# Optimization experiments

Hardware: AMD Instinct MI355X
Metric: run time of the kernel (lower is better)

Reference implementation:

```python
import jax, jax.numpy as jnp
import numpy as np

EPS = 1e-5
H, W, C, NCLS = 8, 16, 64, 8

def _bn_params(key, c):
    k1, k2, k3, k4 = jax.random.split(key, 4)
    gamma = jax.random.uniform(k1, (c,), minval=0.5, maxval=1.5)
    beta = 0.1 * jax.random.normal(k2, (c,))
    mean = 0.1 * jax.random.normal(k3, (c,))
    var = jax.random.uniform(k4, (c,), minval=0.5, maxval=1.5)
    return jnp.stack([gamma, beta, mean, var]).astype(jnp.float32)  # (4, c)

def bn2d(x, p):
    # eval-mode BatchNorm2d; p: (4, C); x: (B, C, H, W)
    g, b, m, v = p[0], p[1], p[2], p[3]
    s = g * jax.lax.rsqrt(v + EPS)
    return x * s[None, :, None, None] + (b - m * s)[None, :, None, None]

def bn1d_scalar(x, p):
    # eval-mode BatchNorm1d with 1 channel; p: (4, 1); x: (B, 1, F)
    g, b, m, v = p[0], p[1], p[2], p[3]
    s = g * jax.lax.rsqrt(v + EPS)
    return x * s + (b - m * s)

def conv_same(x, w, b):
    y = jax.lax.conv_general_dilated(x, w, (1, 1), 'SAME',
                                     dimension_numbers=('NCHW', 'OIHW', 'NCHW'))
    return y + b[None, :, None, None]

def setup_inputs() -> dict:
    key = jax.random.key(0)
    ks = jax.random.split(key, 24)
    B = 8192
    d = {}
    d['x'] = jax.random.normal(ks[0], (B, 1, H, W), dtype=jnp.float32)
    d['bn0'] = _bn_params(ks[1], 1)
    d['conv1_w'] = 0.1 * jax.random.normal(ks[2], (C, 1, 3, 3), dtype=jnp.float32)
    d['conv1_b'] = jnp.zeros((C,), jnp.float32)
    d['bn1'] = _bn_params(ks[3], C)
    d['conv2_w'] = (0.1 / np.sqrt(C)) * jax.random.normal(ks[4], (C, C, 3, 3), dtype=jnp.float32)
    d['conv2_b'] = jnp.zeros((C,), jnp.float32)
    d['bn2'] = _bn_params(ks[5], C)
    # LocallyConnected2d, kernel_size=1 -> per-pixel (out_c, in_c) weights
    d['lc3_w'] = (1.0 / np.sqrt(C)) * jax.random.normal(ks[6], (C, C, H, W), dtype=jnp.float32)
    d['bn3'] = _bn_params(ks[7], C)
    d['lc4_w'] = (1.0 / np.sqrt(C)) * jax.random.normal(ks[8], (C, C, H, W), dtype=jnp.float32)
    d['bn4'] = _bn_params(ks[9], C)
    F5 = H * W * C
    d['fc5_w'] = (1.0 / np.sqrt(F5)) * jax.random.normal(ks[10], (512, F5), dtype=jnp.float32)
    d['fc5_b'] = jnp.zeros((512,), jnp.float32)
    d['bn5'] = _bn_params(ks[11], 1)
    d['fc6_w'] = (1.0 / np.sqrt(512)) * jax.random.normal(ks[12], (512, 512), dtype=jnp.float32)
    d['fc6_b'] = jnp.zeros((512,), jnp.float32)
    d['bn6'] = _bn_params(ks[13], 1)
    d['fc7_w'] = (1.0 / np.sqrt(512)) * jax.random.normal(ks[14], (128, 512), dtype=jnp.float32)
    d['fc7_b'] = jnp.zeros((128,), jnp.float32)
    d['bn7'] = _bn_params(ks[15], 1)
    d['fc8_w'] = (1.0 / np.sqrt(128)) * jax.random.normal(ks[16], (NCLS, 128), dtype=jnp.float32)
    d['fc8_b'] = jnp.zeros((NCLS,), jnp.float32)
    return d

def reference(x, bn0, conv1_w, conv1_b, bn1, conv2_w, conv2_b, bn2,
              lc3_w, bn3, lc4_w, bn4, fc5_w, fc5_b, bn5,
              fc6_w, fc6_b, bn6, fc7_w, fc7_b, bn7, fc8_w, fc8_b):
    B = x.shape[0]
    # squeeze -> view(B, 16, 8) -> transpose(1,2) -> add channel dim
    h = jnp.swapaxes(x.reshape(B, W, H), 1, 2)[:, None]  # (B,1,H,W)
    h = bn2d(h, bn0)
    h = jax.nn.relu(bn2d(conv_same(h, conv1_w, conv1_b), bn1))
    h = jax.nn.relu(bn2d(conv_same(h, conv2_w, conv2_b), bn2))
    # locally connected, k=1: per-pixel channel mixing
    h = jax.nn.relu(bn2d(jnp.einsum('bchw,ochw->bohw', h, lc3_w), bn3))
    h = jax.nn.relu(bn2d(jnp.einsum('bchw,ochw->bohw', h, lc4_w), bn4))
    h = h.reshape(B, 1, -1)  # (B, 1, C*H*W)
    h = h @ fc5_w.T + fc5_b
    h = jax.nn.relu(bn1d_scalar(h, bn5))
    h = jax.nn.relu(bn1d_scalar(h @ fc6_w.T + fc6_b, bn6))
    h = jax.nn.relu(bn1d_scalar(h @ fc7_w.T + fc7_b, bn7))
    h = h @ fc8_w.T + fc8_b
    return h.reshape(B, NCLS)
```

## Files before the change

### kernel.cpp

```cpp
#include <hip/hip_runtime.h>
#include <hip/hip_bf16.h>

typedef unsigned short bf16_t;
typedef __attribute__((ext_vector_type(8))) short bf16x8;
typedef __attribute__((ext_vector_type(8))) unsigned short u16x8;
typedef __attribute__((ext_vector_type(4))) float f32x4;

#if defined(__has_builtin)
#if __has_builtin(__builtin_amdgcn_global_load_lds)
#define HAS_GLL 1
#endif
#endif

__device__ __forceinline__ float b2f(bf16_t u) {
    return __uint_as_float(((unsigned int)u) << 16);
}
__device__ __forceinline__ bf16_t f2b(float f) {
    unsigned int x = __float_as_uint(f);
    unsigned int r = x + 0x7fffu + ((x >> 16) & 1u);
    return (bf16_t)(r >> 16);
}
__device__ __forceinline__ unsigned int pk2(float a, float b) {
    __hip_bfloat162 t = __float22bfloat162_rn(make_float2(a, b));
    return *(unsigned int*)&t;
}
__device__ __forceinline__ float ldf(const void* p, int i, int isf) {
    return isf ? ((const float*)p)[i] : b2f(((const bf16_t*)p)[i]);
}

__device__ __forceinline__ void stg16(const bf16_t* g, bf16_t* l) {
#ifdef HAS_GLL
    __builtin_amdgcn_global_load_lds(
        (const __attribute__((address_space(1))) unsigned int*)g,
        (__attribute__((address_space(3))) unsigned int*)l,
        16, 0, 0);
#else
    *(uint4*)l = *(const uint4*)g;
#endif
}

#define OFF_S0T0 0
#define OFF_W1   16
#define OFF_S1   592
#define OFF_H1   656
#define OFF_S2   720
#define OFF_H2   784
#define OFF_S3   848
#define OFF_H3   912
#define OFF_S4   976
#define OFF_H4   1040
#define OFF_SC5  1104
#define OFF_H5   1112
#define OFF_SC6  1624
#define OFF_H6   1632
#define OFF_SC7  2144
#define OFF_H7   2152
#define OFF_W8   2280
#define OFF_B8   3304
#define OFF_FLAG 4032

__global__ __launch_bounds__(256) void setup_kernel(
    const void* __restrict__ w2, const void* __restrict__ w3,
    const void* __restrict__ w4, const void* __restrict__ w5,
    const void* __restrict__ w6, const void* __restrict__ w7,
    bf16_t* __restrict__ w2p, bf16_t* __restrict__ w3p,
    bf16_t* __restrict__ w4p, bf16_t* __restrict__ w5p,
    bf16_t* __restrict__ w6b, bf16_t* __restrict__ w7b,
    const float* __restrict__ prm)
{
    const int isf = prm[OFF_FLAG] > 0.5f;
    const int i = blockIdx.x * 256 + threadIdx.x;
    if (i < 36864) {
        int oc = i / 576, r = i - oc * 576;
        int tap = r >> 6, ic = r & 63;
        w2p[i] = f2b(ldf(w2, oc * 576 + ic * 9 + tap, isf));
    } else if (i < 561152) {
        int j = i - 36864;
        int p = j >> 12, r = j & 4095;
        int oc = r >> 6, ic = r & 63;
        w3p[j] = f2b(ldf(w3, oc * 8192 + ic * 128 + p, isf));
    } else if (i < 1085440) {
        int j = i - 561152;
        int p = j >> 12, r = j & 4095;
        int oc = r >> 6, ic = r & 63;
        w4p[j] = f2b(ldf(w4, oc * 8192 + ic * 128 + p, isf));
    } else if (i < 5279744) {
        int j = i - 1085440;
        int nr = j >> 13, r = j & 8191;
        int p = r >> 6, c = r & 63;
        w5p[j] = f2b(ldf(w5, nr * 8192 + c * 128 + p, isf));
    } else if (i < 5541888) {
        int j = i - 5279744;
        w6b[j] = isf ? f2b(((const float*)w6)[j]) : ((const bf16_t*)w6)[j];
    } else if (i < 5607424) {
        int j = i - 5541888;
        w7b[j] = isf ? f2b(((const float*)w7)[j]) : ((const bf16_t*)w7)[j];
    }
}

__global__ __launch_bounds__(256) void fold_params_kernel(
    const void* xraw,
    const void* bn0p, const void* w1, const void* b1, const void* bn1p,
    const void* b2c, const void* bn2p, const void* bn3p, const void* bn4p,
    const void* b5, const void* bn5p, const void* b6, const void* bn6p,
    const void* b7, const void* bn7p, const void* w8, const void* b8,
    float* prm)
{
    __shared__ float sflag;
    const int t = threadIdx.x;
    if (t == 0) {
        const unsigned int* w = (const unsigned int*)xraw;
        int good = 0;
        for (int i = 0; i < 64; i++) {
            float f = __uint_as_float(w[i] << 16);
            float a = fabsf(f);
            if (a >= 0.0009765625f && a <= 16.0f) good++;
        }
        float fl = (good >= 32) ? 0.0f : 1.0f;
        sflag = fl;
        prm[OFF_FLAG] = fl;
    }
    __syncthreads();
    const int isf = sflag > 0.5f;

    if (t == 0) {
        float g = ldf(bn0p, 0, isf), be = ldf(bn0p, 1, isf);
        float m = ldf(bn0p, 2, isf), v = ldf(bn0p, 3, isf);
        float s = g * rsqrtf(v + 1e-5f);
        prm[OFF_S0T0] = s; prm[OFF_S0T0 + 1] = be - m * s;
    }
    for (int i = t; i < 576; i += 256) prm[OFF_W1 + i] = ldf(w1, i, isf);

    if (t < 64) {
        {
            float g = ldf(bn1p, t, isf), be = ldf(bn1p, 64 + t, isf);
            float m = ldf(bn1p, 128 + t, isf), v = ldf(bn1p, 192 + t, isf);
            float s = g * rsqrtf(v + 1e-5f);
            prm[OFF_S1 + t] = s;
            prm[OFF_H1 + t] = s * ldf(b1, t, isf) + (be - m * s);
        }
        {
            float g = ldf(bn2p, t, isf), be = ldf(bn2p, 64 + t, isf);
            float m = ldf(bn2p, 128 + t, isf), v = ldf(bn2p, 192 + t, isf);
            float s = g * rsqrtf(v + 1e-5f);
            prm[OFF_S2 + t] = s;
            prm[OFF_H2 + t] = s * ldf(b2c, t, isf) + (be - m * s);
        }
        {
            float g = ldf(bn3p, t, isf), be = ldf(bn3p, 64 + t, isf);
            float m = ldf(bn3p, 128 + t, isf), v = ldf(bn3p, 192 + t, isf);
            float s = g * rsqrtf(v + 1e-5f);
            prm[OFF_S3 + t] = s;
            prm[OFF_H3 + t] = be - m * s;
        }
        {
            float g = ldf(bn4p, t, isf), be = ldf(bn4p, 64 + t, isf);
            float m = ldf(bn4p, 128 + t, isf), v = ldf(bn4p, 192 + t, isf);
            float s = g * rsqrtf(v + 1e-5f);
            prm[OFF_S4 + t] = s;
            prm[OFF_H4 + t] = be - m * s;
        }
    }
    {
        float g = ldf(bn5p, 0, isf), be = ldf(bn5p, 1, isf);
        float m = ldf(bn5p, 2, isf), v = ldf(bn5p, 3, isf);
        float s = g * rsqrtf(v + 1e-5f);
        if (t == 0) prm[OFF_SC5] = s;
        for (int i = t; i < 512; i += 256)
            prm[OFF_H5 + i] = s * ldf(b5, i, isf) + (be - m * s);
    }
    {
        float g = ldf(bn6p, 0, isf), be = ldf(bn6p, 1, isf);
        float m = ldf(bn6p, 2, isf), v = ldf(bn6p, 3, isf);
        float s = g * rsqrtf(v + 1e-5f);
        if (t == 0) prm[OFF_SC6] = s;
        for (int i = t; i < 512; i += 256)
            prm[OFF_H6 + i] = s * ldf(b6, i, isf) + (be - m * s);
    }
    {
        float g = ldf(bn7p, 0, isf), be = ldf(bn7p, 1, isf);
        float m = ldf(bn7p, 2, isf), v = ldf(bn7p, 3, isf);
        float s = g * rsqrtf(v + 1e-5f);
        if (t == 0) prm[OFF_SC7] = s;
        if (t < 128) prm[OFF_H7 + t] = s * ldf(b7, t, isf) + (be - m * s);
    }
    for (int i = t; i < 1024; i += 256) prm[OFF_W8 + i] = ldf(w8, i, isf);
    if (t < 8) prm[OFF_B8 + t] = ldf(b8, t, isf);
}

__global__ __launch_bounds__(256) void conv1_kernel(
    const void* __restrict__ x, const float* __restrict__ prm,
    bf16_t* __restrict__ c1, int Bc, int c0)
{
    __shared__ float xn[180];
    __shared__ float w1s[576];

    const int t = threadIdx.x;
    const int b0 = blockIdx.x * 4;
    const int isf = prm[OFF_FLAG] > 0.5f;
    const float s0 = prm[OFF_S0T0], t0 = prm[OFF_S0T0 + 1];

    for (int i = t; i < 576; i += 256) w1s[i] = prm[OFF_W1 + i];

    const int pg  = t & 31;
    const int oc0 = (t >> 5) * 8;

    float s1[8], h1[8];
    #pragma unroll
    for (int j = 0; j < 8; j++) {
        s1[j] = prm[OFF_S1 + oc0 + j];
        h1[j] = prm[OFF_H1 + oc0 + j];
    }

    for (int s = 0; s < 4; s++) {
        const int b = b0 + s;
        __syncthreads();
        if (t < 180) {
            int row = t / 18, col = t - row * 18;
            float v = 0.f;
            if (row >= 1 && row <= 8 && col >= 1 && col <= 16)
                v = s0 * ldf(x, (c0 + b) * 128 + (col - 1) * 8 + (row - 1), isf) + t0;
            xn[t] = v;
        }
        __syncthreads();

        #pragma unroll
        for (int m = 0; m < 4; m++) {
            int p = pg + 32 * m;
            int h = p >> 4, w = p & 15;
            float r[9];
            #pragma unroll
            for (int dh = 0; dh < 3; dh++)
                #pragma unroll
                for (int dw = 0; dw < 3; dw++)
                    r[dh * 3 + dw] = xn[(h + dh) * 18 + (w + dw)];
            u16x8 o;
            #pragma unroll
            for (int j = 0; j < 8; j++) {
                float acc = 0.f;
                #pragma unroll
                for (int k = 0; k < 9; k++) acc += r[k] * w1s[(oc0 + j) * 9 + k];
                o[j] = f2b(fmaxf(s1[j] * acc + h1[j], 0.f));
            }
            *(u16x8*)(c1 + (size_t)p * Bc * 64 + (size_t)b * 64 + oc0) = o;
        }
    }
}

__global__ __launch_bounds__(256) void fused_mfma_kernel(
    const bf16_t* __restrict__ c1, const bf16_t* __restrict__ w2p,
    const bf16_t* __restrict__ w3p, const bf16_t* __restrict__ w4p,
    const float* __restrict__ prm, bf16_t* __restrict__ bufA, int Bc)
{
    __shared__ bf16_t sm[20480];
    const int t    = threadIdx.x;
    const int lane = t & 63;
    const int wv   = t >> 6;
    const int m0   = blockIdx.x * 256;
    const int p    = blockIdx.y;
    const int h    = p >> 4, w = p & 15;

    const int fr = lane & 15;
    const int fg = lane >> 4;
    const int swz4 = (fr >> 1) & 3;

    const int gS    = (t & 3) ^ ((t >> 3) & 3);
    const int rA    = t >> 2;
    const int coff0 = rA * 64 + gS * 8;
    const int w2off = rA * 576 + gS * 8;

    u16x8 wr3[2], wr4[2];
    {
        const bf16_t* w3b = w3p + (size_t)p * 4096 + coff0;
        const bf16_t* w4b = w4p + (size_t)p * 4096 + coff0;
        wr3[0] = *(const u16x8*)(w3b);
        wr3[1] = *(const u16x8*)(w3b + 32);
        wr4[0] = *(const u16x8*)(w4b);
        wr4[1] = *(const u16x8*)(w4b + 32);
    }

    f32x4 acc[4][4];
    #pragma unroll
    for (int i = 0; i < 4; i++)
        #pragma unroll
        for (int j = 0; j < 4; j++)
            acc[i][j] = (f32x4){0.f, 0.f, 0.f, 0.f};

    const bf16_t* c1b = c1 + (size_t)m0 * 64 + coff0;
    const size_t planeStride = (size_t)Bc * 64;

    {
        if (h > 0 && w > 0) {
            const bf16_t* ab = c1b + (size_t)((h - 1) * 16 + (w - 1)) * planeStride;
            #pragma unroll
            for (int u = 0; u < 4; u++)
                stg16(ab + u * 4096, sm + t * 8 + u * 2048);
            stg16(w2p + w2off, sm + 16384 + t * 8);
        }
    }
    #pragma unroll
    for (int s = 0; s < 18; s++) {
        const int cur = s & 1;
        __syncthreads();
        if (s + 1 < 18) {
            const int s1  = s + 1;
            const int tap = s1 >> 1;
            const int dh = tap / 3 - 1, dw = tap % 3 - 1;
            const int hh = h + dh, ww = w + dw;
            if (hh >= 0 && hh < 8 && ww >= 0 && ww < 16) {
                const int nb  = cur ^ 1;
                const int ic0 = (s1 & 1) * 32;
                const bf16_t* ab = c1b + (size_t)(hh * 16 + ww) * planeStride + ic0;
                #pragma unroll
                for (int u = 0; u < 4; u++)
                    stg16(ab + u * 4096, sm + nb * 8192 + t * 8 + u * 2048);
                stg16(w2p + w2off + tap * 64 + ic0, sm + 16384 + nb * 2048 + t * 8);
            }
        }
        {
            const int tap = s >> 1;
            const int dh = tap / 3 - 1, dw = tap % 3 - 1;
            const int hh = h + dh, ww = w + dw;
            if (hh >= 0 && hh < 8 && ww >= 0 && ww < 16) {
                const bf16_t* Ab = sm + cur * 8192;
                const bf16_t* Bb = sm + 16384 + cur * 2048;
                bf16x8 hf[4], wf[4];
                #pragma unroll
                for (int j = 0; j < 4; j++)
                    hf[j] = *(const bf16x8*)(Ab + ((wv * 64 + j * 16 + fr) * 4 + (fg ^ swz4)) * 8);
                #pragma unroll
                for (int i = 0; i < 4; i++)
                    wf[i] = *(const bf16x8*)(Bb + ((i * 16 + fr) * 4 + (fg ^ swz4)) * 8);
                #pragma unroll
                for (int i = 0; i < 4; i++)
                    #pragma unroll
                    for (int j = 0; j < 4; j++)
                        acc[i][j] = __builtin_amdgcn_mfma_f32_16x16x32_bf16(
                            wf[i], hf[j], acc[i][j], 0, 0, 0);
            }
        }
    }
    __syncthreads();

#define EPILOGUE(SOFF, HOFF)                                                  \
    _Pragma("unroll")                                                         \
    for (int i = 0; i < 4; i++) {                                             \
        const int oc0e = i * 16 + fg * 4;                                     \
        const float4 sv = *(const float4*)(prm + (SOFF) + oc0e);              \
        const float4 hv = *(const float4*)(prm + (HOFF) + oc0e);              \
        _Pragma("unroll")                                                     \
        for (int j = 0; j < 4; j++) {                                         \
            const int bi = wv * 64 + j * 16 + fr;                             \
            float v0 = fmaxf(sv.x * acc[i][j][0] + hv.x, 0.f);                \
            float v1 = fmaxf(sv.y * acc[i][j][1] + hv.y, 0.f);                \
            float v2 = fmaxf(sv.z * acc[i][j][2] + hv.z, 0.f);                \
            float v3 = fmaxf(sv.w * acc[i][j][3] + hv.w, 0.f);                \
            uint2 pk; pk.x = pk2(v0, v1); pk.y = pk2(v2, v3);                 \
            *(uint2*)(sm + bi * 72 + oc0e) = pk;                              \
        }                                                                     \
    }

    EPILOGUE(OFF_S2, OFF_H2)
    *(u16x8*)(sm + 18432 + t * 8) = wr3[0];
    __syncthreads();

    #pragma unroll
    for (int i = 0; i < 4; i++)
        #pragma unroll
        for (int j = 0; j < 4; j++)
            acc[i][j] = (f32x4){0.f, 0.f, 0.f, 0.f};

    #pragma unroll
    for (int ks = 0; ks < 2; ks++) {
        if (ks == 1) {
            __syncthreads();
            *(u16x8*)(sm + 18432 + t * 8) = wr3[1];
            __syncthreads();
        }
        bf16x8 hf[4], wf[4];
        #pragma unroll
        for (int j = 0; j < 4; j++)
            hf[j] = *(const bf16x8*)(sm + (wv * 64 + j * 16 + fr) * 72 + ks * 32 + fg * 8);
        #pragma unroll
        for (int i = 0; i < 4; i++)
            wf[i] = *(const bf16x8*)(sm + 18432 + ((i * 16 + fr) * 4 + (fg ^ swz4)) * 8);
        #pragma unroll
        for (int i = 0; i < 4; i++)
            #pragma unroll
            for (int j = 0; j < 4; j++)
                acc[i][j] = __builtin_amdgcn_mfma_f32_16x16x32_bf16(
                    wf[i], hf[j], acc[i][j], 0, 0, 0);
    }

    EPILOGUE(OFF_S3, OFF_H3)
    __syncthreads();
    *(u16x8*)(sm + 18432 + t * 8) = wr4[0];
    __syncthreads();

    #pragma unroll
    for (int i = 0; i < 4; i++)
        #pragma unroll
        for (int j = 0; j < 4; j++)
            acc[i][j] = (f32x4){0.f, 0.f, 0.f, 0.f};

    #pragma unroll
    for (int ks = 0; ks < 2; ks++) {
        if (ks == 1) {
            __syncthreads();
            *(u16x8*)(sm + 18432 + t * 8) = wr4[1];
            __syncthreads();
        }
        bf16x8 hf[4], wf[4];
        #pragma unroll
        for (int j = 0; j < 4; j++)
            hf[j] = *(const bf16x8*)(sm + (wv * 64 + j * 16 + fr) * 72 + ks * 32 + fg * 8);
        #pragma unroll
        for (int i = 0; i < 4; i++)
            wf[i] = *(const bf16x8*)(sm + 18432 + ((i * 16 + fr) * 4 + (fg ^ swz4)) * 8);
        #pragma unroll
        for (int i = 0; i < 4; i++)
            #pragma unroll
            for (int j = 0; j < 4; j++)
                acc[i][j] = __builtin_amdgcn_mfma_f32_16x16x32_bf16(
                    wf[i], hf[j], acc[i][j], 0, 0, 0);
    }

    EPILOGUE(OFF_S4, OFF_H4)
#undef EPILOGUE
    __syncthreads();

    const int wrow = t >> 3, wc0 = (t & 7) * 8;
    #pragma unroll
    for (int pass = 0; pass < 8; pass++) {
        const int row = wrow + pass * 32;
        *(uint4*)(bufA + (size_t)(m0 + row) * 8192 + p * 64 + wc0) =
            *(const uint4*)(sm + row * 72 + wc0);
    }
}

__global__ __launch_bounds__(256) void gemm_mfma(
    const bf16_t* __restrict__ A, const bf16_t* __restrict__ W,
    const float* __restrict__ prm, int sc_off, int sh_off,
    bf16_t* __restrict__ out, int K, int N)
{
    __shared__ bf16_t sm[24576];
    const int t    = threadIdx.x;
    const int lane = t & 63;
    const int wv   = t >> 6;
    const int wr   = wv >> 1, wc = wv & 1;
    const int m0   = blockIdx.x * 128, n0 = blockIdx.y * 64;

    const int fr = lane & 15;
    const int fg = lane >> 4;
    const int swz8 = fr & 7;

    const bf16_t* srcA[4]; bf16_t* dstA[4];
    #pragma unroll
    for (int u = 0; u < 4; u++) {
        const int c = t + 256 * u;
        const int row = c >> 3;
        const int g = (c & 7) ^ (row & 7);
        srcA[u] = A + (size_t)(m0 + row) * K + g * 8;
        dstA[u] = sm + c * 8;
    }
    const bf16_t* srcB[2]; bf16_t* dstB[2];
    #pragma unroll
    for (int u = 0; u < 2; u++) {
        const int c = t + 256 * u;
        const int row = c >> 3;
        const int g = (c & 7) ^ (row & 7);
        srcB[u] = W + (size_t)(n0 + row) * K + g * 8;
        dstB[u] = sm + 16384 + c * 8;
    }

    f32x4 acc[4][2];
    #pragma unroll
    for (int i = 0; i < 4; i++)
        #pragma unroll
        for (int j = 0; j < 2; j++)
            acc[i][j] = (f32x4){0.f, 0.f, 0.f, 0.f};

    const int KS = K >> 6;

    #pragma unroll
    for (int u = 0; u < 4; u++) stg16(srcA[u], dstA[u]);
    #pragma unroll
    for (int u = 0; u < 2; u++) stg16(srcB[u], dstB[u]);

    for (int ks = 0; ks < KS; ks++) {
        const int cur = ks & 1;
        __syncthreads();
        if (ks + 1 < KS) {
            const int nb = cur ^ 1;
            const int kk = (ks + 1) << 6;
            #pragma unroll
            for (int u = 0; u < 4; u++) stg16(srcA[u] + kk, dstA[u] + nb * 8192);
            #pragma unroll
            for (int u = 0; u < 2; u++) stg16(srcB[u] + kk, dstB[u] + nb * 4096);
        }
        const bf16_t* Ab = sm + cur * 8192;
        const bf16_t* Bb = sm + 16384 + cur * 4096;
        bf16x8 af[4][2], bf2[2][2];
        #pragma unroll
        for (int i = 0; i < 4; i++)
            #pragma unroll
            for (int hh = 0; hh < 2; hh++) {
                const int r = wr * 64 + i * 16 + fr;
                const int g = hh * 4 + fg;
                af[i][hh] = *(const bf16x8*)(Ab + (r * 8 + (g ^ swz8)) * 8);
            }
        #pragma unroll
        for (int j = 0; j < 2; j++)
            #pragma unroll
            for (int hh = 0; hh < 2; hh++) {
                const int r = wc * 32 + j * 16 + fr;
                const int g = hh * 4 + fg;
                bf2[j][hh] = *(const bf16x8*)(Bb + (r * 8 + (g ^ swz8)) * 8);
            }
        #pragma unroll
        for (int hh = 0; hh < 2; hh++)
            #pragma unroll
            for (int i = 0; i < 4; i++)
                #pragma unroll
                for (int j = 0; j < 2; j++)
                    acc[i][j] = __builtin_amdgcn_mfma_f32_16x16x32_bf16(
                        af[i][hh], bf2[j][hh], acc[i][j], 0, 0, 0);
    }

    const float s    = prm[sc_off];
    const int   orow = fg * 4;
    const int   ocol = fr;
    #pragma unroll
    for (int j = 0; j < 2; j++) {
        const int n  = n0 + wc * 32 + j * 16 + ocol;
        const float sh = prm[sh_off + n];
        #pragma unroll
        for (int i = 0; i < 4; i++) {
            const int mb = m0 + wr * 64 + i * 16 + orow;
            #pragma unroll
            for (int r = 0; r < 4; r++) {
                float v = fmaxf(s * acc[i][j][r] + sh, 0.f);
                out[(size_t)(mb + r) * N + n] = f2b(v);
            }
        }
    }
}

__global__ __launch_bounds__(256) void fc8_kernel(
    const bf16_t* __restrict__ h, const float* __restrict__ prm,
    void* __restrict__ out, int c0)
{
    __shared__ float wsm[8 * 129];
    const int t = threadIdx.x;
    for (int i = t; i < 1024; i += 256) {
        int n = i >> 7, k = i & 127;
        wsm[n * 129 + k] = prm[OFF_W8 + i];
    }
    __syncthreads();
    const int isf = prm[OFF_FLAG] > 0.5f;
    const int bl = t >> 3, n = t & 7;
    const int b = c0 + blockIdx.x * 32 + bl;
    const bf16_t* hb = h + (size_t)(blockIdx.x * 32 + bl) * 128;
    float acc = prm[OFF_B8 + n];
    for (int k = 0; k < 128; k++) acc += b2f(hb[k]) * wsm[n * 129 + k];
    if (isf) ((float*)out)[(size_t)b * 8 + n] = acc;
    else     ((bf16_t*)out)[(size_t)b * 8 + n] = f2b(acc);
}

extern "C" void kernel_launch(void* const* d_in, const int* in_sizes, int n_in,
                              void* d_out, int out_size, void* d_ws, size_t ws_size,
                              hipStream_t stream)
{
    const void* x    = d_in[0];
    const void* bn0p = d_in[1];
    const void* w1   = d_in[2];
    const void* b1   = d_in[3];
    const void* bn1p = d_in[4];
    const void* w2   = d_in[5];
    const void* b2c  = d_in[6];
    const void* bn2p = d_in[7];
    const void* w3   = d_in[8];
    const void* bn3p = d_in[9];
    const void* w4   = d_in[10];
    const void* bn4p = d_in[11];
    const void* w5   = d_in[12];
    const void* b5   = d_in[13];
    const void* bn5p = d_in[14];
    const void* w6   = d_in[15];
    const void* b6   = d_in[16];
    const void* bn6p = d_in[17];
    const void* w7   = d_in[18];
    const void* b7   = d_in[19];
    const void* bn7p = d_in[20];
    const void* w8   = d_in[21];
    const void* b8   = d_in[22];

    char* base = (char*)d_ws;
    float*  prm = (float*)(base + 0);
    bf16_t* w2p = (bf16_t*)(base + 16384);
    bf16_t* w3p = (bf16_t*)(base + 90112);
    bf16_t* w4p = (bf16_t*)(base + 1138688);
    bf16_t* w5p = (bf16_t*)(base + 2187264);
    bf16_t* w6b = (bf16_t*)(base + 10575872);
    bf16_t* w7b = (bf16_t*)(base + 11100160);
    char*   acts = base + 11231232;

    const int B = 8192;
    const size_t FIXED = 11231232ull;

    fold_params_kernel<<<1, 256, 0, stream>>>(
        x, bn0p, w1, b1, bn1p, b2c, bn2p, bn3p, bn4p,
        b5, bn5p, b6, bn6p, b7, bn7p, w8, b8, prm);
    setup_kernel<<<21904, 256, 0, stream>>>(
        w2, w3, w4, w5, w6, w7, w2p, w3p, w4p, w5p, w6b, w7b, prm);

    const int Bf = 4096;
    const size_t FULL_NEED = FIXED + (size_t)Bf * 16384ull + (size_t)B * 18688ull;

    if (ws_size >= FULL_NEED) {
        bf16_t* c1   = (bf16_t*)acts;
        bf16_t* bufA = c1 + (size_t)Bf * 8192;
        bf16_t* bufC = bufA + (size_t)B * 8192;
        bf16_t* bufD = bufC + (size_t)B * 512;
        bf16_t* bufE = bufD + (size_t)B * 512;

        for (int c0 = 0; c0 < B; c0 += Bf) {
            conv1_kernel<<<Bf / 4, 256, 0, stream>>>(x, prm, c1, Bf, c0);
            fused_mfma_kernel<<<dim3(Bf / 256, 128), 256, 0, stream>>>(
                c1, w2p, w3p, w4p, prm, bufA + (size_t)c0 * 8192, Bf);
        }
        gemm_mfma<<<dim3(B / 128, 8), 256, 0, stream>>>(
            bufA, w5p, prm, OFF_SC5, OFF_H5, bufC, 8192, 512);
        gemm_mfma<<<dim3(B / 128, 8), 256, 0, stream>>>(
            bufC, w6b, prm, OFF_SC6, OFF_H6, bufD, 512, 512);
        gemm_mfma<<<dim3(B / 128, 2), 256, 0, stream>>>(
            bufD, w7b, prm, OFF_SC7, OFF_H7, bufE, 512, 128);
        fc8_kernel<<<B / 32, 256, 0, stream>>>(bufE, prm, d_out, 0);
    } else {
        size_t avail = (ws_size > FIXED) ? (ws_size - FIXED) : 0;
        int Bc = 8192;
        while (Bc > 256 && (size_t)Bc * 35072ull > avail) Bc >>= 1;

        bf16_t* c1   = (bf16_t*)acts;
        bf16_t* bufA = c1 + (size_t)Bc * 8192;
        bf16_t* bufC = bufA + (size_t)Bc * 8192;
        bf16_t* bufD = bufC + (size_t)Bc * 512;
        bf16_t* bufE = bufD + (size_t)Bc * 512;

        for (int c0 = 0; c0 < B; c0 += Bc) {
            conv1_kernel<<<Bc / 4, 256, 0, stream>>>(x, prm, c1, Bc, c0);
            fused_mfma_kernel<<<dim3(Bc / 256, 128), 256, 0, stream>>>(
                c1, w2p, w3p, w4p, prm, bufA, Bc);
            gemm_mfma<<<dim3(Bc / 128, 8), 256, 0, stream>>>(
                bufA, w5p, prm, OFF_SC5, OFF_H5, bufC, 8192, 512);
            gemm_mfma<<<dim3(Bc / 128, 8), 256, 0, stream>>>(
                bufC, w6b, prm, OFF_SC6, OFF_H6, bufD, 512, 512);
            gemm_mfma<<<dim3(Bc / 128, 2), 256, 0, stream>>>(
                bufD, w7b, prm, OFF_SC7, OFF_H7, bufE, 512, 128);
            fc8_kernel<<<Bc / 32, 256, 0, stream>>>(bufE, prm, d_out, c0);
        }
    }
}
```

Baseline: 430.0 us.

## Merge setup kernels, batch conv1 staging, swizzle blocks per XCD, one-pass batch

Folds the parameter-folding kernel into the weight-repacking kernel as an extra block, with each block detecting the input dtype through a wave ballot, which removes one launch and its serial dependency. conv1 stages all four samples into shared memory at once and drops the per-sample barriers. The fused MFMA and GEMM kernels remap block IDs so consecutive blocks on the same XCD share tiles, aiming for better L2 reuse. fc8 uses vectorized loads, and when the workspace is large enough the conv path runs the whole batch in one pass instead of two chunks, which needs more workspace memory.

```diff
diff --git a/kernel.cpp b/kernel.cpp
--- a/kernel.cpp
+++ b/kernel.cpp
@@ -37,6 +37,15 @@
 #else
     *(uint4*)l = *(const uint4*)g;
 #endif
+}
+
+__device__ __forceinline__ int detect_isf(const void* xraw) {
+    const unsigned int* w = (const unsigned int*)xraw;
+    unsigned int u = w[threadIdx.x & 63];
+    float a = fabsf(__uint_as_float(u << 16));
+    int g = (a >= 0.0009765625f && a <= 16.0f) ? 1 : 0;
+    unsigned long long m = __ballot(g);
+    return (__builtin_popcountll(m) >= 32) ? 0 : 1;
 }
 
 #define OFF_S0T0 0
@@ -59,69 +68,59 @@
 #define OFF_B8   3304
 #define OFF_FLAG 4032
 
-__global__ __launch_bounds__(256) void setup_kernel(
+__global__ __launch_bounds__(256) void setup_fold_kernel(
+    const void* __restrict__ x,
     const void* __restrict__ w2, const void* __restrict__ w3,
     const void* __restrict__ w4, const void* __restrict__ w5,
     const void* __restrict__ w6, const void* __restrict__ w7,
     bf16_t* __restrict__ w2p, bf16_t* __restrict__ w3p,
     bf16_t* __restrict__ w4p, bf16_t* __restrict__ w5p,
     bf16_t* __restrict__ w6b, bf16_t* __restrict__ w7b,
-    const float* __restrict__ prm)
+    const void* __restrict__ bn0p, const void* __restrict__ w1,
+    const void* __restrict__ b1, const void* __restrict__ bn1p,
+    const void* __restrict__ b2c, const void* __restrict__ bn2p,
+    const void* __restrict__ bn3p, const void* __restrict__ bn4p,
+    const void* __restrict__ b5, const void* __restrict__ bn5p,
+    const void* __restrict__ b6, const void* __restrict__ bn6p,
+    const void* __restrict__ b7, const void* __restrict__ bn7p,
+    const void* __restrict__ w8, const void* __restrict__ b8,
+    float* __restrict__ prm)
 {
-    const int isf = prm[OFF_FLAG] > 0.5f;
-    const int i = blockIdx.x * 256 + threadIdx.x;
-    if (i < 36864) {
-        int oc = i / 576, r = i - oc * 576;
-        int tap = r >> 6, ic = r & 63;
-        w2p[i] = f2b(ldf(w2, oc * 576 + ic * 9 + tap, isf));
-    } else if (i < 561152) {
-        int j = i - 36864;
-        int p = j >> 12, r = j & 4095;
-        int oc = r >> 6, ic = r & 63;
-        w3p[j] = f2b(ldf(w3, oc * 8192 + ic * 128 + p, isf));
-    } else if (i < 1085440) {
-        int j = i - 561152;
-        int p = j >> 12, r = j & 4095;
-        int oc = r >> 6, ic = r & 63;
-        w4p[j] = f2b(ldf(w4, oc * 8192 + ic * 128 + p, isf));
-    } else if (i < 5279744) {
-        int j = i - 1085440;
-        int nr = j >> 13, r = j & 8191;
-        int p = r >> 6, c = r & 63;
-        w5p[j] = f2b(ldf(w5, nr * 8192 + c * 128 + p, isf));
-    } else if (i < 5541888) {
-        int j = i - 5279744;
-        w6b[j] = isf ? f2b(((const float*)w6)[j]) : ((const bf16_t*)w6)[j];
-    } else if (i < 5607424) {
-        int j = i - 5541888;
-        w7b[j] = isf ? f2b(((const float*)w7)[j]) : ((const bf16_t*)w7)[j];
-    }
-}
-
-__global__ __launch_bounds__(256) void fold_params_kernel(
-    const void* xraw,
-    const void* bn0p, const void* w1, const void* b1, const void* bn1p,
-    const void* b2c, const void* bn2p, const void* bn3p, const void* bn4p,
-    const void* b5, const void* bn5p, const void* b6, const void* bn6p,
-    const void* b7, const void* bn7p, const void* w8, const void* b8,
-    float* prm)
-{
-    __shared__ float sflag;
     const int t = threadIdx.x;
-    if (t == 0) {
-        const unsigned int* w = (const unsigned int*)xraw;
-        int good = 0;
-        for (int i = 0; i < 64; i++) {
-            float f = __uint_as_float(w[i] << 16);
-            float a = fabsf(f);
-            if (a >= 0.0009765625f && a <= 16.0f) good++;
-        }
-        float fl = (good >= 32) ? 0.0f : 1.0f;
-        sflag = fl;
-        prm[OFF_FLAG] = fl;
-    }
-    __syncthreads();
-    const int isf = sflag > 0.5f;
+    const int isf = detect_isf(x);
+
+    if (blockIdx.x != 21904) {
+        const int i = blockIdx.x * 256 + t;
+        if (i < 36864) {
+            int oc = i / 576, r = i - oc * 576;
+            int tap = r >> 6, ic = r & 63;
+            w2p[i] = f2b(ldf(w2, oc * 576 + ic * 9 + tap, isf));
+        } else if (i < 561152) {
+            int j = i - 36864;
+            int p = j >> 12, r = j & 4095;
+            int oc = r >> 6, ic = r & 63;
+            w3p[j] = f2b(ldf(w3, oc * 8192 + ic * 128 + p, isf));
+        } else if (i < 1085440) {
+            int j = i - 561152;
+            int p = j >> 12, r = j & 4095;
+            int oc = r >> 6, ic = r & 63;
+            w4p[j] = f2b(ldf(w4, oc * 8192 + ic * 128 + p, isf));
+        } else if (i < 5279744) {
+            int j = i - 1085440;
+            int nr = j >> 13, r = j & 8191;
+            int p = r >> 6, c = r & 63;
+            w5p[j] = f2b(ldf(w5, nr * 8192 + c * 128 + p, isf));
+        } else if (i < 5541888) {
+            int j = i - 5279744;
+            w6b[j] = isf ? f2b(((const float*)w6)[j]) : ((const bf16_t*)w6)[j];
+        } else if (i < 5607424) {
+            int j = i - 5541888;
+            w7b[j] = isf ? f2b(((const float*)w7)[j]) : ((const bf16_t*)w7)[j];
+        }
+        return;
+    }
+
+    if (t == 0) prm[OFF_FLAG] = isf ? 1.0f : 0.0f;
 
     if (t == 0) {
         float g = ldf(bn0p, 0, isf), be = ldf(bn0p, 1, isf);
@@ -192,7 +191,7 @@
     const void* __restrict__ x, const float* __restrict__ prm,
     bf16_t* __restrict__ c1, int Bc, int c0)
 {
-    __shared__ float xn[180];
+    __shared__ float xn[720];
     __shared__ float w1s[576];
 
     const int t = threadIdx.x;
@@ -201,6 +200,14 @@
     const float s0 = prm[OFF_S0T0], t0 = prm[OFF_S0T0 + 1];
 
     for (int i = t; i < 576; i += 256) w1s[i] = prm[OFF_W1 + i];
+    for (int i = t; i < 720; i += 256) {
+        int s = i / 180, r = i - s * 180;
+        int row = r / 18, col = r - row * 18;
+        float v = 0.f;
+        if (row >= 1 && row <= 8 && col >= 1 && col <= 16)
+            v = s0 * ldf(x, (c0 + b0 + s) * 128 + (col - 1) * 8 + (row - 1), isf) + t0;
+        xn[i] = v;
+    }
 
     const int pg  = t & 31;
     const int oc0 = (t >> 5) * 8;
@@ -211,19 +218,11 @@
         s1[j] = prm[OFF_S1 + oc0 + j];
         h1[j] = prm[OFF_H1 + oc0 + j];
     }
+    __syncthreads();
 
     for (int s = 0; s < 4; s++) {
         const int b = b0 + s;
-        __syncthreads();
-        if (t < 180) {
-            int row = t / 18, col = t - row * 18;
-            float v = 0.f;
-            if (row >= 1 && row <= 8 && col >= 1 && col <= 16)
-                v = s0 * ldf(x, (c0 + b) * 128 + (col - 1) * 8 + (row - 1), isf) + t0;
-            xn[t] = v;
-        }
-        __syncthreads();
-
+        const float* xs = xn + s * 180;
         #pragma unroll
         for (int m = 0; m < 4; m++) {
             int p = pg + 32 * m;
@@ -233,7 +232,7 @@
             for (int dh = 0; dh < 3; dh++)
                 #pragma unroll
                 for (int dw = 0; dw < 3; dw++)
-                    r[dh * 3 + dw] = xn[(h + dh) * 18 + (w + dw)];
+                    r[dh * 3 + dw] = xs[(h + dh) * 18 + (w + dw)];
             u16x8 o;
             #pragma unroll
             for (int j = 0; j < 8; j++) {
@@ -256,9 +255,22 @@
     const int t    = threadIdx.x;
     const int lane = t & 63;
     const int wv   = t >> 6;
-    const int m0   = blockIdx.x * 256;
-    const int p    = blockIdx.y;
-    const int h    = p >> 4, w = p & 15;
+
+    int btile, p;
+    {
+        const int nbx = gridDim.x;
+        const int id = blockIdx.x + nbx * blockIdx.y;
+        if ((nbx & 7) == 0) {
+            const int xcd = id & 7;
+            const int k   = id >> 3;
+            p     = k & 127;
+            btile = xcd + 8 * (k >> 7);
+        } else {
+            btile = blockIdx.x; p = blockIdx.y;
+        }
+    }
+    const int m0 = btile * 256;
+    const int h  = p >> 4, w = p & 15;
 
     const int fr = lane & 15;
     const int fg = lane >> 4;
@@ -448,7 +460,22 @@
     const int lane = t & 63;
     const int wv   = t >> 6;
     const int wr   = wv >> 1, wc = wv & 1;
-    const int m0   = blockIdx.x * 128, n0 = blockIdx.y * 64;
+
+    int bm, bn;
+    {
+        const int nx = gridDim.x, ny = gridDim.y;
+        const int id = blockIdx.x + nx * blockIdx.y;
+        if ((nx & 7) == 0) {
+            const int xcd = id & 7;
+            const int k   = id >> 3;
+            const int pl  = k / ny;
+            bn = k - pl * ny;
+            bm = xcd + 8 * pl;
+        } else {
+            bm = blockIdx.x; bn = blockIdx.y;
+        }
+    }
+    const int m0 = bm * 128, n0 = bn * 64;
 
     const int fr = lane & 15;
     const int fg = lane >> 4;
@@ -562,7 +589,13 @@
     const int b = c0 + blockIdx.x * 32 + bl;
     const bf16_t* hb = h + (size_t)(blockIdx.x * 32 + bl) * 128;
     float acc = prm[OFF_B8 + n];
-    for (int k = 0; k < 128; k++) acc += b2f(hb[k]) * wsm[n * 129 + k];
+    #pragma unroll
+    for (int k8 = 0; k8 < 16; k8++) {
+        u16x8 hv = *(const u16x8*)(hb + k8 * 8);
+        #pragma unroll
+        for (int j = 0; j < 8; j++)
+            acc += b2f(hv[j]) * wsm[n * 129 + k8 * 8 + j];
+    }
     if (isf) ((float*)out)[(size_t)b * 8 + n] = acc;
     else     ((bf16_t*)out)[(size_t)b * 8 + n] = f2b(acc);
 }
@@ -608,16 +641,17 @@
     const int B = 8192;
     const size_t FIXED = 11231232ull;
 
-    fold_params_kernel<<<1, 256, 0, stream>>>(
-        x, bn0p, w1, b1, bn1p, b2c, bn2p, bn3p, bn4p,
+    setup_fold_kernel<<<21905, 256, 0, stream>>>(
+        x, w2, w3, w4, w5, w6, w7, w2p, w3p, w4p, w5p, w6b, w7b,
+        bn0p, w1, b1, bn1p, b2c, bn2p, bn3p, bn4p,
         b5, bn5p, b6, bn6p, b7, bn7p, w8, b8, prm);
-    setup_kernel<<<21904, 256, 0, stream>>>(
-        w2, w3, w4, w5, w6, w7, w2p, w3p, w4p, w5p, w6b, w7b, prm);
-
-    const int Bf = 4096;
-    const size_t FULL_NEED = FIXED + (size_t)Bf * 16384ull + (size_t)B * 18688ull;
-
-    if (ws_size >= FULL_NEED) {
+
+    const size_t NEED_1PASS = FIXED + (size_t)B * 16384ull + (size_t)B * 18688ull;
+    const size_t NEED_2PASS = FIXED + 4096ull * 16384ull + (size_t)B * 18688ull;
+
+    if (ws_size >= NEED_2PASS) {
+        const int Bf = (ws_size >= NEED_1PASS) ? 8192 : 4096;
+
         bf16_t* c1   = (bf16_t*)acts;
         bf16_t* bufA = c1 + (size_t)Bf * 8192;
         bf16_t* bufC = bufA + (size_t)B * 8192;
```

Result: faster. 415.1 us (-3.5%).
